# Kernel tuning notes

Hardware: AMD Instinct MI355X
Metric: run time of the kernel (lower is better)

Reference implementation:

```python
import jax, jax.numpy as jnp
import numpy as np

N = 50000      # nodes
E = 800000     # edges (avg degree 16)
DIN = 128
DOUT = 128
L = 8          # num GCN2Conv layers
ALPHA = 0.1
THETA = 0.5


def setup_inputs() -> dict:
    key = jax.random.key(0)
    ks = jax.random.split(key, 5)
    x = jax.random.normal(ks[0], (N, DIN), jnp.float32)
    edge_index = jax.random.randint(ks[1], (2, E), 0, N, dtype=jnp.int64)
    # pre-normalized adjacency weights (normalize=False in GCN2Conv -> adj_t already normalized)
    edge_weight = jax.random.uniform(ks[2], (E,), jnp.float32) / 16.0
    W_lin = jax.random.normal(ks[3], (DIN, DOUT), jnp.float32) / np.sqrt(DIN).astype(np.float32)
    b_lin = jnp.zeros((DOUT,), jnp.float32)
    W_convs = jax.random.normal(ks[4], (L, DOUT, DOUT), jnp.float32) / np.sqrt(DOUT).astype(np.float32)
    return {"x": x, "edge_weight": edge_weight, "W_lin": W_lin, "b_lin": b_lin,
            "W_convs": W_convs, "edge_index": edge_index}


def reference(x, edge_weight, W_lin, b_lin, W_convs, edge_index):
    src, dst = edge_index[0], edge_index[1]
    # betas for GCN2Conv layer l (1-indexed): beta_l = log(theta/l + 1)
    betas = np.log(THETA / np.arange(1, L + 1) + 1.0).astype(np.float32)
    # x = lins(x).relu(); dropout p=0 is a no-op
    x0 = jax.nn.relu(x @ W_lin + b_lin)          # [N, DOUT]
    h = x0
    for l in range(L):
        # sparse propagate: agg = A @ h  (SpMM via gather + segment_sum)
        agg = jax.ops.segment_sum(h[src] * edge_weight[:, None], dst, num_segments=N)
        # initial-residual mixing
        m = (1.0 - ALPHA) * agg + ALPHA * x0
        # identity mapping (shared_weights): out = (1-beta)*m + beta*(m @ W)
        h = jax.nn.relu((1.0 - betas[l]) * m + betas[l] * (m @ W_convs[l]))
    return h
```

## Files before the change

### kernel.cpp

```cpp
#include <hip/hip_runtime.h>
#include <math.h>

#define N_NODES 50000
#define N_EDGES 800000
#define DIM 128
#define PAD 120

#define EPB 2048
#define NBLKA 391
#define BIN_SHIFT 8
#define NBIN 196
#define HISTW 197

typedef __attribute__((ext_vector_type(8))) short short8;
typedef __attribute__((ext_vector_type(4))) float floatx4;

__device__ __forceinline__ unsigned short f32_to_bf16(float f) {
    unsigned int u = __float_as_uint(f);
    u += 0x7fffu + ((u >> 16) & 1u);
    return (unsigned short)(u >> 16);
}
__device__ __forceinline__ float bf16_to_f32(unsigned short h) {
    return __uint_as_float((unsigned int)h << 16);
}

__device__ __forceinline__ int swz(int row, int blk) {
    return row * 128 + (((blk ^ (row & 7)) & 15) << 3);
}

__global__ __launch_bounds__(256) void prep(const float* __restrict__ Wlin,
                                            const float* __restrict__ Wcv,
                                            unsigned short* __restrict__ WTg) {
    int i = blockIdx.x * 256 + threadIdx.x;
    int m = i >> 14;
    int n = (i >> 7) & 127;
    int k = i & 127;
    float v;
    if (m == 0) {
        v = Wlin[k * 128 + n];
    } else {
        int l = m - 1;
        float beta = logf(0.5f / (float)(l + 1) + 1.0f);
        v = beta * Wcv[(size_t)l * 16384 + k * 128 + n]
            + ((n == k) ? (1.0f - beta) : 0.0f);
    }
    WTg[i] = f32_to_bf16(v);
}

__global__ __launch_bounds__(256) void bin_sort(const int* __restrict__ src,
                                                const int* __restrict__ dst,
                                                const float* __restrict__ ew,
                                                int* __restrict__ histg,
                                                int2* __restrict__ binbuf) {
    __shared__ int hist[NBIN];
    __shared__ int base[NBIN + 1];
    __shared__ int cur[NBIN];
    __shared__ int2 sorted[EPB];
    int tid = threadIdx.x;
    int e0 = blockIdx.x * EPB;
    if (tid < NBIN) hist[tid] = 0;
    __syncthreads();
    for (int i = tid; i < EPB; i += 256) {
        int e = e0 + i;
        if (e < N_EDGES) atomicAdd(&hist[dst[e] >> BIN_SHIFT], 1);
    }
    __syncthreads();
    if (tid < NBIN) base[tid + 1] = hist[tid];
    if (tid == 0) base[0] = 0;
    __syncthreads();
    for (int off = 1; off < NBIN + 1; off <<= 1) {
        int v = 0;
        if (tid >= off && tid <= NBIN) v = base[tid - off];
        __syncthreads();
        if (tid >= off && tid <= NBIN) base[tid] += v;
        __syncthreads();
    }
    if (tid < NBIN) cur[tid] = base[tid];
    __syncthreads();
    for (int i = tid; i < EPB; i += 256) {
        int e = e0 + i;
        if (e < N_EDGES) {
            int d = dst[e];
            int pos = atomicAdd(&cur[d >> BIN_SHIFT], 1);
            int2 p;
            p.x = (src[e] & 0xFFFF) | (d << 16);
            p.y = __float_as_int(ew[e]);
            sorted[pos] = p;
        }
    }
    __syncthreads();
    int total = base[NBIN];
    for (int k = tid; k < total; k += 256)
        binbuf[(size_t)blockIdx.x * EPB + k] = sorted[k];
    if (tid <= NBIN) histg[blockIdx.x * HISTW + tid] = base[tid];
}

__global__ __launch_bounds__(512) void bin_scatter(const int* __restrict__ histg,
                                                   const int2* __restrict__ binbuf,
                                                   int* __restrict__ cnt,
                                                   int2* __restrict__ bucket) {
    __shared__ int segstart[NBLKA];
    __shared__ int pref[NBLKA + 1];
    __shared__ int c[128];
    int bin = blockIdx.x >> 1;
    int half = blockIdx.x & 1;
    int tid = threadIdx.x;
    if (tid < 128) c[tid] = 0;
    if (tid < NBLKA) {
        int bs = histg[tid * HISTW + bin];
        int be = histg[tid * HISTW + bin + 1];
        segstart[tid] = tid * EPB + bs;
        pref[tid + 1] = be - bs;
    }
    if (tid == 0) pref[0] = 0;
    __syncthreads();
    for (int off = 1; off < NBLKA + 1; off <<= 1) {
        int v = 0;
        if (tid >= off && tid <= NBLKA) v = pref[tid - off];
        __syncthreads();
        if (tid >= off && tid <= NBLKA) pref[tid] += v;
        __syncthreads();
    }
    int T = pref[NBLKA];
    for (int idx = tid; idx < T; idx += 512) {
        int lo = 0, hi = NBLKA - 1;
        while (lo < hi) {
            int mid = (lo + hi + 1) >> 1;
            if (pref[mid] <= idx) lo = mid; else hi = mid - 1;
        }
        int2 p = binbuf[(size_t)segstart[lo] + (idx - pref[lo])];
        int d = ((unsigned)p.x) >> 16;
        int dloc = d & ((1 << BIN_SHIFT) - 1);
        if ((dloc >> 7) == half) {
            int pos = atomicAdd(&c[dloc & 127], 1);
            if (pos < PAD) {
                int2 q; q.x = p.x & 0xFFFF; q.y = p.y;
                bucket[(size_t)d * PAD + pos] = q;
            }
        }
    }
    __syncthreads();
    int node0 = (bin << BIN_SHIFT) + (half << 7);
    if (tid < 128 && node0 + tid < N_NODES)
        cnt[node0 + tid] = min(c[tid], PAD);
}

__global__ __launch_bounds__(256) void gemm_x0(const float* __restrict__ x,
                                               const unsigned short* __restrict__ WTg,
                                               const float* __restrict__ bias,
                                               unsigned short* __restrict__ x0B) {
    __shared__ unsigned short WT[128][136];
    for (int idx = threadIdx.x; idx < 2048; idx += 256) {
        int n = idx >> 4, c = idx & 15;
        *(short8*)(void*)&WT[n][c * 8] =
            *(const short8*)(const void*)(WTg + n * 128 + c * 8);
    }
    __syncthreads();
    int wave = threadIdx.x >> 6;
    int lane = threadIdx.x & 63;
    int r0 = (blockIdx.x * 4 + wave) * 16;
    if (r0 >= N_NODES) return;
    int mrow = lane & 15;
    int quad = lane >> 4;
    floatx4 acc[8];
#pragma unroll
    for (int t = 0; t < 8; t++) acc[t] = {0.f, 0.f, 0.f, 0.f};
#pragma unroll
    for (int k0 = 0; k0 < 128; k0 += 32) {
        const float* arow = x + (size_t)(r0 + mrow) * DIM;
        floatx4 alo = *(const floatx4*)(const void*)(arow + k0 + quad * 8);
        floatx4 ahi = *(const floatx4*)(const void*)(arow + k0 + quad * 8 + 4);
        short8 a;
#pragma unroll
        for (int j = 0; j < 4; j++) a[j] = (short)f32_to_bf16(alo[j]);
#pragma unroll
        for (int j = 0; j < 4; j++) a[4 + j] = (short)f32_to_bf16(ahi[j]);
#pragma unroll
        for (int t = 0; t < 8; t++) {
            short8 b = *(const short8*)(const void*)(&WT[t * 16 + mrow][k0 + quad * 8]);
            acc[t] = __builtin_amdgcn_mfma_f32_16x16x32_bf16(a, b, acc[t], 0, 0, 0);
        }
    }
#pragma unroll
    for (int t = 0; t < 8; t++) {
        int col = t * 16 + mrow;
        float bv = bias[col];
#pragma unroll
        for (int i = 0; i < 4; i++) {
            int row = r0 + quad * 4 + i;
            float v = fmaxf(acc[t][i] + bv, 0.f);
            x0B[(size_t)row * DIM + col] = f32_to_bf16(v);
        }
    }
}

__global__ __launch_bounds__(512, 4) void layer_fused(
        const unsigned short* __restrict__ hB,
        const unsigned short* __restrict__ x0B,
        const int* __restrict__ cnt,
        const int2* __restrict__ bucket,
        const unsigned short* __restrict__ WTg,
        float* __restrict__ outF,
        unsigned short* __restrict__ outB) {
    __shared__ unsigned short WT[128 * 128];
    __shared__ unsigned short M[32 * 128];
    int tid = threadIdx.x;
    for (int idx = tid; idx < 2048; idx += 512) {
        int n = idx >> 4, c = idx & 15;
        *(short8*)(void*)&WT[swz(n, c)] =
            *(const short8*)(const void*)(WTg + n * 128 + c * 8);
    }
    int wave = tid >> 6;
    int lane = tid & 63;
    int eg = lane >> 4;
    int fb = (lane & 15) * 8;
    int r0 = blockIdx.x * 32;

    for (int s = 0; s < 4; s++) {
        int row = (wave << 2) + s;
        int node = r0 + row;
        float acc[8] = {0.f, 0.f, 0.f, 0.f, 0.f, 0.f, 0.f, 0.f};
        if (node < N_NODES) {
            int end = min(cnt[node], PAD);
            if (end > 0) {
                const int2* ep = bucket + (size_t)node * PAD;
                int last = end - 1;
                for (int i = 0; i < end; i += 16) {
                    int i0 = i + eg, i1 = i0 + 4, i2 = i0 + 8, i3 = i0 + 12;
                    int2 e0 = ep[min(i0, last)];
                    int2 e1 = ep[min(i1, last)];
                    int2 e2 = ep[min(i2, last)];
                    int2 e3 = ep[min(i3, last)];
                    short8 r0v = *(const short8*)(const void*)(hB + (size_t)e0.x * DIM + fb);
                    short8 r1v = *(const short8*)(const void*)(hB + (size_t)e1.x * DIM + fb);
                    short8 r2v = *(const short8*)(const void*)(hB + (size_t)e2.x * DIM + fb);
                    short8 r3v = *(const short8*)(const void*)(hB + (size_t)e3.x * DIM + fb);
                    float w0 = (i0 < end) ? __int_as_float(e0.y) : 0.f;
                    float w1 = (i1 < end) ? __int_as_float(e1.y) : 0.f;
                    float w2 = (i2 < end) ? __int_as_float(e2.y) : 0.f;
                    float w3 = (i3 < end) ? __int_as_float(e3.y) : 0.f;
#pragma unroll
                    for (int j = 0; j < 8; j++) {
                        acc[j] = fmaf(w0, bf16_to_f32((unsigned short)r0v[j]), acc[j]);
                        acc[j] = fmaf(w1, bf16_to_f32((unsigned short)r1v[j]), acc[j]);
                        acc[j] = fmaf(w2, bf16_to_f32((unsigned short)r2v[j]), acc[j]);
                        acc[j] = fmaf(w3, bf16_to_f32((unsigned short)r3v[j]), acc[j]);
                    }
                }
            }
        }
#pragma unroll
        for (int j = 0; j < 8; j++) {
            acc[j] += __shfl_down(acc[j], 32);
            acc[j] += __shfl_down(acc[j], 16);
        }
        if (lane < 16) {
            short8 o;
            if (node < N_NODES) {
                short8 xv = *(const short8*)(const void*)(x0B + (size_t)node * DIM + fb);
#pragma unroll
                for (int j = 0; j < 8; j++)
                    o[j] = (short)f32_to_bf16(0.9f * acc[j]
                                              + 0.1f * bf16_to_f32((unsigned short)xv[j]));
            } else {
#pragma unroll
                for (int j = 0; j < 8; j++) o[j] = 0;
            }
            *(short8*)(void*)&M[swz(row, lane & 15)] = o;
        }
    }
    __syncthreads();

    int mrow = lane & 15;
    int quad = lane >> 4;
    int rt = wave >> 2;
    int ctb = (wave & 3) * 2;
    floatx4 acc2[2];
    acc2[0] = {0.f, 0.f, 0.f, 0.f};
    acc2[1] = {0.f, 0.f, 0.f, 0.f};
#pragma unroll
    for (int k0 = 0; k0 < 128; k0 += 32) {
        short8 a = *(const short8*)(const void*)(&M[swz(rt * 16 + mrow, k0 / 8 + quad)]);
#pragma unroll
        for (int t = 0; t < 2; t++) {
            short8 b = *(const short8*)(const void*)(&WT[swz((ctb + t) * 16 + mrow, k0 / 8 + quad)]);
            acc2[t] = __builtin_amdgcn_mfma_f32_16x16x32_bf16(a, b, acc2[t], 0, 0, 0);
        }
    }
#pragma unroll
    for (int t = 0; t < 2; t++) {
        int col = (ctb + t) * 16 + mrow;
#pragma unroll
        for (int i = 0; i < 4; i++) {
            int row = r0 + rt * 16 + quad * 4 + i;
            if (row < N_NODES) {
                float v = fmaxf(acc2[t][i], 0.f);
                size_t off = (size_t)row * DIM + col;
                if (outF) outF[off] = v;
                if (outB) outB[off] = f32_to_bf16(v);
            }
        }
    }
}


extern "C" void kernel_launch(void* const* d_in, const int* in_sizes, int n_in,
                              void* d_out, int out_size, void* d_ws, size_t ws_size,
                              hipStream_t stream) {
    const float* x    = (const float*)d_in[0];
    const float* ew   = (const float*)d_in[1];
    const float* Wlin = (const float*)d_in[2];
    const float* blin = (const float*)d_in[3];
    const float* Wcv  = (const float*)d_in[4];
    const int* eidx = (const int*)d_in[5];
    const int* esrc = eidx;
    const int* edst = eidx + N_EDGES;
    float* out = (float*)d_out;

    char* ws = (char*)d_ws;
    unsigned short* x0B = (unsigned short*)(ws);
    unsigned short* hA  = (unsigned short*)(ws + 12800000);
    unsigned short* hB2 = (unsigned short*)(ws + 25600000);
    int* cnt            = (int*)(ws + 38400000);
    int2* bucket        = (int2*)(ws + 38600064);
    unsigned short* WTg = (unsigned short*)(ws + 86600064);
    int* histg          = (int*)(ws + 86894976);
    int2* binbuf        = (int2*)ws;

    prep<<<576, 256, 0, stream>>>(Wlin, Wcv, WTg);

    bin_sort<<<NBLKA, 256, 0, stream>>>(esrc, edst, ew, histg, binbuf);
    bin_scatter<<<NBIN * 2, 512, 0, stream>>>(histg, binbuf, cnt, bucket);

    gemm_x0<<<(N_NODES + 63) / 64, 256, 0, stream>>>(x, WTg, blin, x0B);

    const unsigned short* hin = x0B;
    for (int l = 0; l < 8; l++) {
        unsigned short* hout = (l == 7) ? nullptr : ((l & 1) ? hB2 : hA);
        layer_fused<<<1563, 512, 0, stream>>>(hin, x0B, cnt, bucket,
                                              WTg + (size_t)(1 + l) * 16384,
                                              (l == 7) ? out : nullptr, hout);
        hin = hout;
    }
}
```

Before: 453.5 us.

## Fold weight prep into bin sort and simplify per-bin scatter

Merges the weight-preparation kernel into the edge bin-sort kernel as extra blocks, removing one launch. The sort now uses 1024-edge chunks, which doubles the number of chunk blocks. bin_scatter now runs one 1024-thread block per bin, and each thread walks one chunk's segment in order. That replaces the prefix scan and the per-edge binary search, and ends the duplicated reads across two half-bin blocks. In exchange, threads get uneven serial loops, and the histogram buffer doubles in size inside the workspace.

```diff
diff --git a/kernel.cpp b/kernel.cpp
--- a/kernel.cpp
+++ b/kernel.cpp
@@ -6,11 +6,12 @@
 #define DIM 128
 #define PAD 120
 
-#define EPB 2048
-#define NBLKA 391
+#define EPB 1024
+#define NBLKA 782
 #define BIN_SHIFT 8
 #define NBIN 196
 #define HISTW 197
+#define PREP_BLOCKS 576
 
 typedef __attribute__((ext_vector_type(8))) short short8;
 typedef __attribute__((ext_vector_type(4))) float floatx4;
@@ -28,42 +29,40 @@
     return row * 128 + (((blk ^ (row & 7)) & 15) << 3);
 }
 
-__global__ __launch_bounds__(256) void prep(const float* __restrict__ Wlin,
-                                            const float* __restrict__ Wcv,
-                                            unsigned short* __restrict__ WTg) {
-    int i = blockIdx.x * 256 + threadIdx.x;
-    int m = i >> 14;
-    int n = (i >> 7) & 127;
-    int k = i & 127;
-    float v;
-    if (m == 0) {
-        v = Wlin[k * 128 + n];
-    } else {
-        int l = m - 1;
-        float beta = logf(0.5f / (float)(l + 1) + 1.0f);
-        v = beta * Wcv[(size_t)l * 16384 + k * 128 + n]
-            + ((n == k) ? (1.0f - beta) : 0.0f);
-    }
-    WTg[i] = f32_to_bf16(v);
-}
-
-__global__ __launch_bounds__(256) void bin_sort(const int* __restrict__ src,
+__global__ __launch_bounds__(256) void sortprep(const int* __restrict__ src,
                                                 const int* __restrict__ dst,
                                                 const float* __restrict__ ew,
+                                                const float* __restrict__ Wlin,
+                                                const float* __restrict__ Wcv,
                                                 int* __restrict__ histg,
-                                                int2* __restrict__ binbuf) {
+                                                int2* __restrict__ binbuf,
+                                                unsigned short* __restrict__ WTg) {
+    if (blockIdx.x >= NBLKA) {
+        int i = (blockIdx.x - NBLKA) * 256 + threadIdx.x;
+        int m = i >> 14;
+        int n = (i >> 7) & 127;
+        int k = i & 127;
+        float v;
+        if (m == 0) {
+            v = Wlin[k * 128 + n];
+        } else {
+            int l = m - 1;
+            float beta = logf(0.5f / (float)(l + 1) + 1.0f);
+            v = beta * Wcv[(size_t)l * 16384 + k * 128 + n]
+                + ((n == k) ? (1.0f - beta) : 0.0f);
+        }
+        WTg[i] = f32_to_bf16(v);
+        return;
+    }
     __shared__ int hist[NBIN];
     __shared__ int base[NBIN + 1];
-    __shared__ int cur[NBIN];
     __shared__ int2 sorted[EPB];
     int tid = threadIdx.x;
     int e0 = blockIdx.x * EPB;
+    int n = min(EPB, N_EDGES - e0);
     if (tid < NBIN) hist[tid] = 0;
     __syncthreads();
-    for (int i = tid; i < EPB; i += 256) {
-        int e = e0 + i;
-        if (e < N_EDGES) atomicAdd(&hist[dst[e] >> BIN_SHIFT], 1);
-    }
+    for (int i = tid; i < n; i += 256) atomicAdd(&hist[dst[e0 + i] >> BIN_SHIFT], 1);
     __syncthreads();
     if (tid < NBIN) base[tid + 1] = hist[tid];
     if (tid == 0) base[0] = 0;
@@ -75,64 +74,40 @@
         if (tid >= off && tid <= NBIN) base[tid] += v;
         __syncthreads();
     }
-    if (tid < NBIN) cur[tid] = base[tid];
-    __syncthreads();
-    for (int i = tid; i < EPB; i += 256) {
+    if (tid < NBIN) hist[tid] = base[tid];
+    __syncthreads();
+    for (int i = tid; i < n; i += 256) {
         int e = e0 + i;
-        if (e < N_EDGES) {
-            int d = dst[e];
-            int pos = atomicAdd(&cur[d >> BIN_SHIFT], 1);
-            int2 p;
-            p.x = (src[e] & 0xFFFF) | (d << 16);
-            p.y = __float_as_int(ew[e]);
-            sorted[pos] = p;
-        }
-    }
-    __syncthreads();
-    int total = base[NBIN];
-    for (int k = tid; k < total; k += 256)
+        int d = dst[e];
+        int pos = atomicAdd(&hist[d >> BIN_SHIFT], 1);
+        int2 p;
+        p.x = (src[e] & 0xFFFF) | (d << 16);
+        p.y = __float_as_int(ew[e]);
+        sorted[pos] = p;
+    }
+    __syncthreads();
+    for (int k = tid; k < n; k += 256)
         binbuf[(size_t)blockIdx.x * EPB + k] = sorted[k];
     if (tid <= NBIN) histg[blockIdx.x * HISTW + tid] = base[tid];
 }
 
-__global__ __launch_bounds__(512) void bin_scatter(const int* __restrict__ histg,
-                                                   const int2* __restrict__ binbuf,
-                                                   int* __restrict__ cnt,
-                                                   int2* __restrict__ bucket) {
-    __shared__ int segstart[NBLKA];
-    __shared__ int pref[NBLKA + 1];
-    __shared__ int c[128];
-    int bin = blockIdx.x >> 1;
-    int half = blockIdx.x & 1;
+__global__ __launch_bounds__(1024) void bin_scatter(const int* __restrict__ histg,
+                                                    const int2* __restrict__ binbuf,
+                                                    int* __restrict__ cnt,
+                                                    int2* __restrict__ bucket) {
+    __shared__ int c[256];
+    int bin = blockIdx.x;
     int tid = threadIdx.x;
-    if (tid < 128) c[tid] = 0;
+    if (tid < 256) c[tid] = 0;
+    __syncthreads();
     if (tid < NBLKA) {
         int bs = histg[tid * HISTW + bin];
         int be = histg[tid * HISTW + bin + 1];
-        segstart[tid] = tid * EPB + bs;
-        pref[tid + 1] = be - bs;
-    }
-    if (tid == 0) pref[0] = 0;
-    __syncthreads();
-    for (int off = 1; off < NBLKA + 1; off <<= 1) {
-        int v = 0;
-        if (tid >= off && tid <= NBLKA) v = pref[tid - off];
-        __syncthreads();
-        if (tid >= off && tid <= NBLKA) pref[tid] += v;
-        __syncthreads();
-    }
-    int T = pref[NBLKA];
-    for (int idx = tid; idx < T; idx += 512) {
-        int lo = 0, hi = NBLKA - 1;
-        while (lo < hi) {
-            int mid = (lo + hi + 1) >> 1;
-            if (pref[mid] <= idx) lo = mid; else hi = mid - 1;
-        }
-        int2 p = binbuf[(size_t)segstart[lo] + (idx - pref[lo])];
-        int d = ((unsigned)p.x) >> 16;
-        int dloc = d & ((1 << BIN_SHIFT) - 1);
-        if ((dloc >> 7) == half) {
-            int pos = atomicAdd(&c[dloc & 127], 1);
+        const int2* sp = binbuf + (size_t)tid * EPB;
+        for (int k = bs; k < be; k++) {
+            int2 p = sp[k];
+            int d = ((unsigned)p.x) >> 16;
+            int pos = atomicAdd(&c[d & 255], 1);
             if (pos < PAD) {
                 int2 q; q.x = p.x & 0xFFFF; q.y = p.y;
                 bucket[(size_t)d * PAD + pos] = q;
@@ -140,8 +115,8 @@
         }
     }
     __syncthreads();
-    int node0 = (bin << BIN_SHIFT) + (half << 7);
-    if (tid < 128 && node0 + tid < N_NODES)
+    int node0 = bin << BIN_SHIFT;
+    if (tid < 256 && node0 + tid < N_NODES)
         cnt[node0 + tid] = min(c[tid], PAD);
 }
 
@@ -327,10 +302,10 @@
     int* histg          = (int*)(ws + 86894976);
     int2* binbuf        = (int2*)ws;
 
-    prep<<<576, 256, 0, stream>>>(Wlin, Wcv, WTg);
-
-    bin_sort<<<NBLKA, 256, 0, stream>>>(esrc, edst, ew, histg, binbuf);
-    bin_scatter<<<NBIN * 2, 512, 0, stream>>>(histg, binbuf, cnt, bucket);
+    sortprep<<<NBLKA + PREP_BLOCKS, 256, 0, stream>>>(esrc, edst, ew, Wlin, Wcv,
+                                                      histg, binbuf, WTg);
+
+    bin_scatter<<<NBIN, 1024, 0, stream>>>(histg, binbuf, cnt, bucket);
 
     gemm_x0<<<(N_NODES + 63) / 64, 256, 0, stream>>>(x, WTg, blin, x0B);
 
```

Measured after the change: 450.1 us. About the same (-0.8%).
